# Optimization experiments

Hardware: AMD Instinct MI355X
Metric: run time of the kernel (lower is better)

## Reference

```python
import jax, jax.numpy as jnp
import numpy as np
from jax import lax

V, E, H = 32000, 32, 128
B, T = 8, 256


def setup_inputs() -> dict:
    key = jax.random.key(0)
    ks = jax.random.split(key, 10)
    inv = lambda n: 1.0 / np.sqrt(n)
    return {
        "x": jax.random.randint(ks[0], (B, T), 0, V, dtype=jnp.int32),
        "emb": jax.random.normal(ks[1], (V, E), dtype=jnp.float32),
        "W_attn": jax.random.normal(ks[2], (H, H), dtype=jnp.float32) * inv(H),   # attn_W weight
        "U_attn": jax.random.normal(ks[3], (H, H), dtype=jnp.float32) * inv(H),   # attn_U weight
        "v_attn": jax.random.normal(ks[4], (H,), dtype=jnp.float32) * inv(H),     # attn_v weight
        "W_ih": jax.random.normal(ks[5], (E + H, H), dtype=jnp.float32) * inv(E + H),
        "b_ih": jnp.zeros((H,), dtype=jnp.float32),
        "W_hh": jax.random.normal(ks[6], (H, H), dtype=jnp.float32) * inv(H),
        "b_hh": jnp.zeros((H,), dtype=jnp.float32),
        "W_out": jax.random.normal(ks[7], (H, V), dtype=jnp.float32) * inv(H),
        "b_out": jnp.zeros((V,), dtype=jnp.float32),
    }


def _run(x, emb, W_attn, U_attn, v_attn, W_ih, b_ih, W_hh, b_hh, W_out, b_out):
    Bb, Tt = x.shape
    Hh = W_hh.shape[0]
    embeds = jnp.swapaxes(emb[x], 0, 1)  # [T, B, E]
    t_idx = jnp.arange(Tt)

    def step(carry, inp):
        h, hid_buf = carry            # h: [B,H]; hid_buf: [T,B,H] (rows >= t are zeros)
        e_t, t = inp                  # e_t: [B,E]
        # Bahdanau attention over hidden states from steps < t
        q = h @ W_attn                                   # [B,H]
        keys = hid_buf @ U_attn                          # [T,B,H] (recomputed each step, as in source)
        energy = jnp.tanh(q[None, :, :] + keys)          # [T,B,H]
        scores = jnp.einsum('tbh,h->tb', energy, v_attn) # [T,B]
        valid = (jnp.arange(Tt) < t)[:, None]
        scores = jnp.where(valid, scores, -1e9)
        w = jax.nn.softmax(scores, axis=0)               # [T,B]
        ctx = jnp.einsum('tb,tbh->bh', w, hid_buf)       # [B,H]
        ctx = jnp.where(t > 0, ctx, jnp.zeros_like(ctx)) # t=0: zero context
        rnn_in = jnp.concatenate([e_t, ctx], axis=1)     # [B,E+H]
        h_new = jnp.tanh(rnn_in @ W_ih + b_ih + h @ W_hh + b_hh)
        hid_buf = hid_buf.at[t].set(h_new)
        return (h_new, hid_buf), h_new

    carry0 = (jnp.zeros((Bb, Hh), embeds.dtype), jnp.zeros((Tt, Bb, Hh), embeds.dtype))
    (h_final, _), outs = lax.scan(step, carry0, (embeds, t_idx))
    outputs = jnp.swapaxes(outs, 0, 1)                   # [B,T,H]
    logits = outputs @ W_out + b_out                     # [B,T,V]
    return logits, h_final


def reference(x, emb, W_attn, U_attn, v_attn, W_ih, b_ih, W_hh, b_hh, W_out, b_out):
    return _run(x, emb, W_attn, U_attn, v_attn, W_ih, b_ih, W_hh, b_hh, W_out, b_out)
```

## Files before the change

kernel.cpp:

```cpp
#include <hip/hip_runtime.h>
#include <hip/hip_fp16.h>
#include <hip/hip_bf16.h>
#include <cstdint>

#define TLEN  256
#define HD    128
#define BATCH 8
#define VOCAB 32000
#define EMBD  32
#define ROWB  272

typedef __attribute__((ext_vector_type(8))) short short8v;
typedef __attribute__((ext_vector_type(8))) unsigned short ushort8v;
typedef __attribute__((ext_vector_type(4))) float f32x4;
typedef __attribute__((ext_vector_type(2))) float f32x2;
typedef __attribute__((ext_vector_type(2))) _Float16 hv2;

__device__ __forceinline__ float tanhfast(float x){
  float e = __builtin_amdgcn_exp2f(x * 2.8853900817779268f);
  return 1.0f - 2.0f * __builtin_amdgcn_rcpf(e + 1.0f);
}
__device__ __forceinline__ unsigned short f2bf(float f){
  unsigned u = __float_as_uint(f);
  return (unsigned short)((u + 0x7fffu + ((u >> 16) & 1u)) >> 16);
}
__device__ __forceinline__ float h2f(unsigned short u){
  return __half2float(__ushort_as_half(u));
}
__device__ __forceinline__ unsigned short f2h(float f){
  return __half_as_ushort(__float2half(f));
}
__device__ __forceinline__ unsigned pk2(float lo, float hi){
  return __builtin_bit_cast(unsigned, __floats2half2_rn(lo, hi));
}
__device__ __forceinline__ float fdot2u(unsigned a, unsigned b, float c){
#if __has_builtin(__builtin_amdgcn_fdot2)
  return __builtin_amdgcn_fdot2(__builtin_bit_cast(hv2, a), __builtin_bit_cast(hv2, b), c, false);
#else
  float2 fa = __half22float2(__builtin_bit_cast(__half2, a));
  float2 fb = __half22float2(__builtin_bit_cast(__half2, b));
  return c + fa.x*fb.x + fa.y*fb.y;
#endif
}
__device__ __forceinline__ f32x2 fma2(f32x2 a, f32x2 b, f32x2 c){
#if __has_builtin(__builtin_elementwise_fma)
  return __builtin_elementwise_fma(a, b, c);
#else
  f32x2 r; r.x = fmaf(a.x, b.x, c.x); r.y = fmaf(a.y, b.y, c.y); return r;
#endif
}
__device__ __forceinline__ void ld8u(const void* p, unsigned* d){
  uint4 a = *(const uint4*)p;
  uint4 b = *(const uint4*)((const char*)p + 16);
  d[0]=a.x; d[1]=a.y; d[2]=a.z; d[3]=a.w; d[4]=b.x; d[5]=b.y; d[6]=b.z; d[7]=b.w;
}
__device__ __forceinline__ void gload_lds16(const void* g, void* l){
  __builtin_amdgcn_global_load_lds((const __attribute__((address_space(1))) void*)g,
                                   (__attribute__((address_space(3))) void*)l, 16, 0, 0);
}

__device__ __forceinline__ float dpp_add1(float x){
  int y = __builtin_amdgcn_mov_dpp(__float_as_int(x), 0xB1, 0xF, 0xF, true);
  return x + __int_as_float(y);
}
__device__ __forceinline__ float dpp_add2(float x){
  int y = __builtin_amdgcn_mov_dpp(__float_as_int(x), 0x4E, 0xF, 0xF, true);
  return x + __int_as_float(y);
}
__device__ __forceinline__ float dpp_shl4(float x){
  int y = __builtin_amdgcn_mov_dpp(__float_as_int(x), 0x104, 0xF, 0xF, true);
  return x + __int_as_float(y);
}
__device__ __forceinline__ float dpp_shl8(float x){
  int y = __builtin_amdgcn_mov_dpp(__float_as_int(x), 0x108, 0xF, 0xF, true);
  return x + __int_as_float(y);
}
__device__ __forceinline__ float swz_add4(float x){
  int y = __builtin_amdgcn_ds_swizzle(__float_as_int(x), 0x101F);
  return x + __int_as_float(y);
}
__device__ __forceinline__ float swz_add16(float x){
  int y = __builtin_amdgcn_ds_swizzle(__float_as_int(x), 0x401F);
  return x + __int_as_float(y);
}

#define SCR(s) ((((s) & 15) << 4) | ((s) >> 4))

__global__ void prep_ex_kernel(const int* __restrict__ x, const float* __restrict__ emb,
                               const float* __restrict__ W_ih, const float* __restrict__ b_ih,
                               const float* __restrict__ b_hh, float* __restrict__ ex){
  int bt = blockIdx.x;
  int c  = threadIdx.x;
  int ix = x[bt];
  const float* er = emb + (long)ix * EMBD;
  float acc = b_ih[c] + b_hh[c];
  #pragma unroll
  for (int e = 0; e < EMBD; ++e) acc += er[e] * W_ih[e * HD + c];
  ex[bt * HD + c] = acc;
}

__global__ void prep_wt_kernel(const float* __restrict__ W_out, unsigned short* __restrict__ Wbt){
  __shared__ float tile[32][33];
  int tx = threadIdx.x & 31, ty = threadIdx.x >> 5;
  int n0 = blockIdx.x * 32, k0 = blockIdx.y * 32;
  #pragma unroll
  for (int j = 0; j < 4; ++j){
    int k = ty + j * 8;
    tile[k][tx] = W_out[(long)(k0 + k) * VOCAB + n0 + tx];
  }
  __syncthreads();
  #pragma unroll
  for (int j = 0; j < 4; ++j){
    int n = ty + j * 8;
    Wbt[(long)(n0 + n) * HD + k0 + tx] = f2bf(tile[tx][n]);
  }
}

__launch_bounds__(1024)
__global__ void scan_kernel(const float* __restrict__ W_attn, const float* __restrict__ U_attn,
                            const float* __restrict__ v_attn, const float* __restrict__ W_ih,
                            const float* __restrict__ W_hh, const float* __restrict__ ex,
                            unsigned short* __restrict__ out_bf, float* __restrict__ h_final){
  extern __shared__ char lds[];
  char* keysB = lds;
  char* hWcB  = lds + 69632;
  float* fbuf   = (float*)(lds + 139264);
  float* E_pad    = fbuf;
  float* hh_lds   = fbuf + 160;
  float* scores_e = fbuf + 288;
  unsigned* h_pk  = (unsigned*)(fbuf + 544);

  const int b    = blockIdx.x;
  const int tid  = threadIdx.x;
  const int lane = tid & 63, wv = tid >> 6;
  const int c_   = tid >> 3, rg = tid & 7;
  const int sg   = lane >> 3, cg = lane & 7;
  const int cg3  = cg & 3;
  const int sgx  = sg + 8*(cg >> 2);
  const int cp   = wv*4 + cg3;

  const float LOG2E = 1.4426950408889634f;
  const float C2F   = 2.8853900817779268f;

  if (tid < HD) hh_lds[tid] = 0.f;

  unsigned Wa2[8], Ua2[8], Wh2[8], Wc2[8];
  {
    float* stage = (float*)lds;
    float4* d4 = (float4*)stage;
    {
      const float4* s4 = (const float4*)W_attn;
      for (int i = 0; i < 4; ++i) d4[tid + i*1024] = s4[tid + i*1024];
      __syncthreads();
      #pragma unroll
      for (int i = 0; i < 8; ++i)
        Wa2[i] = pk2(stage[(rg*16 + 2*i)*HD + c_], stage[(rg*16 + 2*i + 1)*HD + c_]);
      __syncthreads();
    }
    {
      const float4* s4 = (const float4*)U_attn;
      for (int i = 0; i < 4; ++i) d4[tid + i*1024] = s4[tid + i*1024];
      __syncthreads();
      #pragma unroll
      for (int i = 0; i < 8; ++i)
        Ua2[i] = pk2(stage[(rg*16 + 2*i)*HD + c_], stage[(rg*16 + 2*i + 1)*HD + c_]);
      __syncthreads();
    }
    {
      const float4* s4 = (const float4*)W_hh;
      for (int i = 0; i < 4; ++i) d4[tid + i*1024] = s4[tid + i*1024];
      __syncthreads();
      #pragma unroll
      for (int i = 0; i < 8; ++i)
        Wh2[i] = pk2(stage[(rg*16 + 2*i)*HD + c_], stage[(rg*16 + 2*i + 1)*HD + c_]);
      __syncthreads();
    }
    {
      const float4* s4 = (const float4*)(W_ih + EMBD*HD);
      for (int i = 0; i < 4; ++i) d4[tid + i*1024] = s4[tid + i*1024];
      __syncthreads();
      #pragma unroll
      for (int i = 0; i < 8; ++i)
        Wc2[i] = pk2(stage[(rg*16 + 2*i)*HD + c_], stage[(rg*16 + 2*i + 1)*HD + c_]);
      __syncthreads();
    }
  }

  {
    float4 z = {0.f, 0.f, 0.f, 0.f};
    float4* hz = (float4*)hWcB;
    hz[tid] = z; hz[tid + 1024] = z; hz[tid + 2048] = z; hz[tid + 3072] = z;
    if (tid < 256) hz[tid + 4096] = z;
    if (tid < 64) ((float4*)scores_e)[tid] = z;
    if (tid < 64) h_pk[tid] = 0u;
  }

  f32x2 v2[8]; float VsumL;
  {
    const float* vg = v_attn + cg*16;
    float s = 0.f;
    #pragma unroll
    for (int i = 0; i < 8; ++i){
      f32x2 vv; vv.x = vg[2*i]; vv.y = vg[2*i+1];
      v2[i] = vv; s += vv.x + vv.y;
    }
    s = dpp_add1(s); s = dpp_add2(s); s = swz_add4(s);
    VsumL = s * LOG2E;
  }

  const float* exb = ex + (long)b * TLEN * HD;

  for (int t = 0; t < TLEN; ++t){
    float2 evpre = *(const float2*)(exb + t*HD + 2*cp);

    if (t > 0){
      {
        unsigned h2u[8];
        ld8u((const char*)h_pk + rg*32, h2u);
        float aq = 0.f, ak = 0.f, ah = 0.f, aw = 0.f;
        #pragma unroll
        for (int i = 0; i < 8; ++i){
          aq = fdot2u(h2u[i], Wa2[i], aq);
          ak = fdot2u(h2u[i], Ua2[i], ak);
          ah = fdot2u(h2u[i], Wh2[i], ah);
          aw = fdot2u(h2u[i], Wc2[i], aw);
        }
        aq = dpp_add1(aq); aq = dpp_add2(aq); aq = dpp_shl4(aq);
        ak = dpp_add1(ak); ak = dpp_add2(ak); ak = dpp_shl4(ak);
        ah = dpp_add1(ah); ah = dpp_add2(ah); ah = dpp_shl4(ah);
        aw = dpp_add1(aw); aw = dpp_add2(aw); aw = dpp_shl4(aw);
        if (rg == 0){
          E_pad[c_ + (c_>>4)*4] = __builtin_amdgcn_exp2f(aq * C2F);
          hh_lds[c_] = ah;
          int s = t - 1;
          float G = fminf(__builtin_amdgcn_exp2f(ak * C2F), 60000.f);
          *(unsigned short*)(keysB + s*ROWB + c_*2) = f2h(G);
          *(unsigned short*)(hWcB  + s*ROWB + c_*2) = f2h(aw);
        }
      }
      __syncthreads();

      {
        f32x2 E2[8];
        {
          const float4* E4 = (const float4*)(E_pad + cg*20);
          #pragma unroll
          for (int i = 0; i < 4; ++i){
            float4 ev = E4[i];
            f32x2 a, bb; a.x = ev.x; a.y = ev.y; bb.x = ev.z; bb.y = ev.w;
            E2[2*i] = a; E2[2*i+1] = bb;
          }
        }
        #pragma unroll
        for (int it = 0; it < 2; ++it){
          int s = wv*8 + sg + it*128;
          if (s < t){
            unsigned gu[8];
            ld8u(keysB + s*ROWB + cg*32, gu);
            f32x2 D[8];
            #pragma unroll
            for (int i = 0; i < 8; ++i){
              hv2 g = __builtin_bit_cast(hv2, gu[i]);
              f32x2 d;
              d.x = fmaf((float)g.x, E2[i].x, 1.0f);
              d.y = fmaf((float)g.y, E2[i].y, 1.0f);
              D[i] = d;
            }
            f32x2 acc2; acc2.x = 0.f; acc2.y = 0.f;
            #pragma unroll
            for (int i = 0; i < 8; i += 2){
              f32x2 p = D[i] * D[i+1];
              float R = __builtin_amdgcn_rcpf(p.x * p.y);
              f32x2 sw = p.yx * R;
              acc2 = fma2(v2[i],   sw * D[i+1], acc2);
              acc2 = fma2(v2[i+1], sw * D[i],   acc2);
            }
            float ac = acc2.x + acc2.y;
            ac = dpp_add1(ac); ac = dpp_add2(ac); ac = dpp_shl4(ac);
            float e = __builtin_amdgcn_exp2f(fmaf(-C2F, ac, VsumL));
            if (cg == 0) scores_e[SCR(s)] = e;
          }
        }
      }
      __syncthreads();
    }

    {
      float a0 = 0.f, a1 = 0.f, es = 0.f;
      const char* pw = hWcB + cp*4 + sgx*ROWB;
      const float* sc = scores_e + sgx*16;
      int jmax = (t - sgx + 15) >> 4;
      for (int j = 0; j < jmax; j += 4){
        float4 e4 = *(const float4*)(sc + j);
        hv2 h0 = __builtin_bit_cast(hv2, *(const unsigned*)(pw));
        hv2 h1 = __builtin_bit_cast(hv2, *(const unsigned*)(pw + 16*ROWB));
        hv2 h2v = __builtin_bit_cast(hv2, *(const unsigned*)(pw + 32*ROWB));
        hv2 h3 = __builtin_bit_cast(hv2, *(const unsigned*)(pw + 48*ROWB));
        es += (e4.x + e4.y) + (e4.z + e4.w);
        a0 = fmaf((float)h0.x, e4.x, a0); a1 = fmaf((float)h0.y, e4.x, a1);
        a0 = fmaf((float)h1.x, e4.y, a0); a1 = fmaf((float)h1.y, e4.y, a1);
        a0 = fmaf((float)h2v.x, e4.z, a0); a1 = fmaf((float)h2v.y, e4.z, a1);
        a0 = fmaf((float)h3.x, e4.w, a0); a1 = fmaf((float)h3.y, e4.w, a1);
        pw += 64*ROWB;
      }
      a0 = dpp_shl4(a0); a0 = dpp_shl8(a0); a0 = swz_add16(a0); a0 += __shfl_xor(a0, 32);
      a1 = dpp_shl4(a1); a1 = dpp_shl8(a1); a1 = swz_add16(a1); a1 += __shfl_xor(a1, 32);
      es = dpp_shl4(es); es = dpp_shl8(es); es = swz_add16(es); es += __shfl_xor(es, 32);
      if (sgx == 0){
        float invZ = __builtin_amdgcn_rcpf(es);
        float cw0 = (t > 0) ? a0 * invZ : 0.f;
        float cw1 = (t > 0) ? a1 * invZ : 0.f;
        int c0 = 2*cp;
        float2 hhv = *(const float2*)(&hh_lds[c0]);
        float h0 = tanhfast(evpre.x + hhv.x + cw0);
        float h1 = tanhfast(evpre.y + hhv.y + cw1);
        h_pk[cp] = pk2(h0, h1);
        unsigned po = (unsigned)f2bf(h0) | ((unsigned)f2bf(h1) << 16);
        *(unsigned*)(&out_bf[((long)b*TLEN + t)*HD + c0]) = po;
        if (t == TLEN-1){ float2 hw = { h0, h1 }; *(float2*)&h_final[b*HD + c0] = hw; }
      }
    }
    __syncthreads();
  }
}

__launch_bounds__(256, 2)
__global__ void gemm_kernel(const unsigned short* __restrict__ A, const unsigned short* __restrict__ Bt,
                            const float* __restrict__ bias, float* __restrict__ C){
  __shared__ char sAB[65536];
  char* sA = sAB;
  char* sB = sAB + 32768;
  const int tid = threadIdx.x;
  const int lane = tid & 63, wv = tid >> 6;
  const int n0 = blockIdx.x * 128, m0 = blockIdx.y * 128;
  const char* Ab = (const char*)A + (long)m0 * 256;
  const char* Bb = (const char*)Bt + (long)n0 * 256;

  #pragma unroll
  for (int it = 0; it < 8; ++it){
    int p  = it*4096 + wv*1024 + lane*16;
    int ps = p ^ (((p >> 8) & 7) << 4);
    gload_lds16(Ab + ps, sA + it*4096 + wv*1024);
    gload_lds16(Bb + ps, sB + it*4096 + wv*1024);
  }
  __syncthreads();

  f32x4 acc[2][8] = {};
  const int r15 = lane & 15, r4 = lane >> 4;
  #pragma unroll
  for (int kk = 0; kk < 4; ++kk){
    short8v af[2], bfr[8];
    #pragma unroll
    for (int mi = 0; mi < 2; ++mi){
      int row = wv*32 + mi*16 + r15;
      int off = row*256 + kk*64 + r4*16;
      af[mi] = *(const short8v*)(sA + (off ^ ((row & 7) << 4)));
    }
    #pragma unroll
    for (int ni = 0; ni < 8; ++ni){
      int row = ni*16 + r15;
      int off = row*256 + kk*64 + r4*16;
      bfr[ni] = *(const short8v*)(sB + (off ^ ((row & 7) << 4)));
    }
    #pragma unroll
    for (int ni = 0; ni < 8; ++ni)
      #pragma unroll
      for (int mi = 0; mi < 2; ++mi)
        acc[mi][ni] = __builtin_amdgcn_mfma_f32_16x16x32_bf16(af[mi], bfr[ni], acc[mi][ni], 0, 0, 0);
  }

  #pragma unroll
  for (int mi = 0; mi < 2; ++mi){
    int rbase = m0 + wv*32 + mi*16 + r4*4;
    #pragma unroll
    for (int ni = 0; ni < 8; ++ni){
      int col = n0 + ni*16 + r15;
      float bv = bias[col];
      #pragma unroll
      for (int j = 0; j < 4; ++j)
        C[(long)(rbase + j) * VOCAB + col] = acc[mi][ni][j] + bv;
    }
  }
}

extern "C" void kernel_launch(void* const* d_in, const int* in_sizes, int n_in,
                              void* d_out, int out_size, void* d_ws, size_t ws_size,
                              hipStream_t stream){
  const int*   x      = (const int*)d_in[0];
  const float* emb    = (const float*)d_in[1];
  const float* W_attn = (const float*)d_in[2];
  const float* U_attn = (const float*)d_in[3];
  const float* v_attn = (const float*)d_in[4];
  const float* W_ih   = (const float*)d_in[5];
  const float* b_ih   = (const float*)d_in[6];
  const float* W_hh   = (const float*)d_in[7];
  const float* b_hh   = (const float*)d_in[8];
  const float* W_out  = (const float*)d_in[9];
  const float* b_out  = (const float*)d_in[10];

  float* logits  = (float*)d_out;
  float* h_final = logits + (long)BATCH * TLEN * VOCAB;

  char* ws = (char*)d_ws;
  float*          ex   = (float*)ws;
  unsigned short* Wbt  = (unsigned short*)(ws + 1048576);
  unsigned short* outb = (unsigned short*)(ws + 1048576 + 8192000);

  prep_ex_kernel<<<BATCH*TLEN, HD, 0, stream>>>(x, emb, W_ih, b_ih, b_hh, ex);
  prep_wt_kernel<<<dim3(VOCAB/32, HD/32), 256, 0, stream>>>(W_out, Wbt);

  const int ldsBytes = 139264 + 608*4;
  hipFuncSetAttribute((const void*)scan_kernel, hipFuncAttributeMaxDynamicSharedMemorySize, ldsBytes);
  scan_kernel<<<BATCH, 1024, ldsBytes, stream>>>(W_attn, U_attn, v_attn, W_ih, W_hh, ex, outb, h_final);

  gemm_kernel<<<dim3(VOCAB/128, (BATCH*TLEN)/128), 256, 0, stream>>>(outb, Wbt, b_out, logits);
}
```

Measured before the change: 650.2 us.

## Fuse scan and output GEMM into one persistent kernel with progress flags

Merges the recurrent scan and the vocabulary projection GEMM into a single launch. Eight blocks run the scan and publish per-batch progress every 64 steps via release atomics. Worker blocks poll these flags and compute GEMM tiles for rows that are already finished, so the large projection overlaps with the serial scan instead of waiting for it. The risks are deadlock if the scan blocks are not scheduled alongside spinning workers, and reduced GEMM efficiency because only 4 of 16 waves per 1024-thread worker block do the math and occupancy is limited by the large LDS allocation.

```diff
diff --git a/kernel.cpp b/kernel.cpp
--- a/kernel.cpp
+++ b/kernel.cpp
@@ -9,6 +9,7 @@
 #define VOCAB 32000
 #define EMBD  32
 #define ROWB  272
+#define NWORK 240
 
 typedef __attribute__((ext_vector_type(8))) short short8v;
 typedef __attribute__((ext_vector_type(8))) unsigned short ushort8v;
@@ -88,9 +89,11 @@
 
 __global__ void prep_ex_kernel(const int* __restrict__ x, const float* __restrict__ emb,
                                const float* __restrict__ W_ih, const float* __restrict__ b_ih,
-                               const float* __restrict__ b_hh, float* __restrict__ ex){
+                               const float* __restrict__ b_hh, float* __restrict__ ex,
+                               int* progress){
   int bt = blockIdx.x;
   int c  = threadIdx.x;
+  if (bt == 0 && c < BATCH) progress[c] = -1;
   int ix = x[bt];
   const float* er = emb + (long)ix * EMBD;
   float acc = b_ih[c] + b_hh[c];
@@ -116,12 +119,11 @@
   }
 }
 
-__launch_bounds__(1024)
-__global__ void scan_kernel(const float* __restrict__ W_attn, const float* __restrict__ U_attn,
-                            const float* __restrict__ v_attn, const float* __restrict__ W_ih,
-                            const float* __restrict__ W_hh, const float* __restrict__ ex,
-                            unsigned short* __restrict__ out_bf, float* __restrict__ h_final){
-  extern __shared__ char lds[];
+__device__ void scan_body(char* lds,
+                          const float* W_attn, const float* U_attn, const float* v_attn,
+                          const float* W_ih, const float* W_hh, const float* ex,
+                          unsigned short* out_bf, float* h_final, int* progress,
+                          int b, int tid){
   char* keysB = lds;
   char* hWcB  = lds + 69632;
   float* fbuf   = (float*)(lds + 139264);
@@ -130,8 +132,6 @@
   float* scores_e = fbuf + 288;
   unsigned* h_pk  = (unsigned*)(fbuf + 544);
 
-  const int b    = blockIdx.x;
-  const int tid  = threadIdx.x;
   const int lane = tid & 63, wv = tid >> 6;
   const int c_   = tid >> 3, rg = tid & 7;
   const int sg   = lane >> 3, cg = lane & 7;
@@ -321,65 +321,101 @@
       }
     }
     __syncthreads();
-  }
-}
-
-__launch_bounds__(256, 2)
-__global__ void gemm_kernel(const unsigned short* __restrict__ A, const unsigned short* __restrict__ Bt,
-                            const float* __restrict__ bias, float* __restrict__ C){
-  __shared__ char sAB[65536];
-  char* sA = sAB;
-  char* sB = sAB + 32768;
-  const int tid = threadIdx.x;
+
+    if (((t & 63) == 63) && tid == 0){
+      __threadfence();
+      __hip_atomic_store(&progress[b], t, __ATOMIC_RELEASE, __HIP_MEMORY_SCOPE_AGENT);
+    }
+  }
+}
+
+__device__ void worker_body(char* lds, const unsigned short* A, const unsigned short* Bt,
+                            const float* bias, float* C, int* progress, int wid, int tid){
+  char* sA = lds;
+  char* sB = lds + 32768;
   const int lane = tid & 63, wv = tid >> 6;
-  const int n0 = blockIdx.x * 128, m0 = blockIdx.y * 128;
-  const char* Ab = (const char*)A + (long)m0 * 256;
-  const char* Bb = (const char*)Bt + (long)n0 * 256;
-
-  #pragma unroll
-  for (int it = 0; it < 8; ++it){
-    int p  = it*4096 + wv*1024 + lane*16;
-    int ps = p ^ (((p >> 8) & 7) << 4);
-    gload_lds16(Ab + ps, sA + it*4096 + wv*1024);
-    gload_lds16(Bb + ps, sB + it*4096 + wv*1024);
-  }
-  __syncthreads();
-
-  f32x4 acc[2][8] = {};
   const int r15 = lane & 15, r4 = lane >> 4;
-  #pragma unroll
-  for (int kk = 0; kk < 4; ++kk){
-    short8v af[2], bfr[8];
-    #pragma unroll
-    for (int mi = 0; mi < 2; ++mi){
-      int row = wv*32 + mi*16 + r15;
-      int off = row*256 + kk*64 + r4*16;
-      af[mi] = *(const short8v*)(sA + (off ^ ((row & 7) << 4)));
-    }
-    #pragma unroll
-    for (int ni = 0; ni < 8; ++ni){
-      int row = ni*16 + r15;
-      int off = row*256 + kk*64 + r4*16;
-      bfr[ni] = *(const short8v*)(sB + (off ^ ((row & 7) << 4)));
-    }
-    #pragma unroll
-    for (int ni = 0; ni < 8; ++ni)
-      #pragma unroll
-      for (int mi = 0; mi < 2; ++mi)
-        acc[mi][ni] = __builtin_amdgcn_mfma_f32_16x16x32_bf16(af[mi], bfr[ni], acc[mi][ni], 0, 0, 0);
-  }
-
-  #pragma unroll
-  for (int mi = 0; mi < 2; ++mi){
-    int rbase = m0 + wv*32 + mi*16 + r4*4;
-    #pragma unroll
-    for (int ni = 0; ni < 8; ++ni){
-      int col = n0 + ni*16 + r15;
-      float bv = bias[col];
-      #pragma unroll
-      for (int j = 0; j < 4; ++j)
-        C[(long)(rbase + j) * VOCAB + col] = acc[mi][ni][j] + bv;
-    }
+
+  for (int tau = wid; tau < 4000; tau += NWORK){
+    int ph  = (tau >= 2000) ? 1 : 0;
+    int r   = tau - ph*2000;
+    int ni  = r >> 3;
+    int mi  = ((r & 7) << 1) + ph;
+    int bb  = mi >> 1;
+    int need = (mi & 1) ? 255 : 127;
+
+    if (tid == 0){
+      while (__hip_atomic_load(&progress[bb], __ATOMIC_ACQUIRE, __HIP_MEMORY_SCOPE_AGENT) < need)
+        __builtin_amdgcn_s_sleep(2);
+    }
+    __syncthreads();
+
+    const int n0 = ni * 128, m0 = mi * 128;
+    if (wv < 4){
+      const char* Ab = (const char*)A + (long)m0 * 256;
+      const char* Bb = (const char*)Bt + (long)n0 * 256;
+      #pragma unroll
+      for (int it = 0; it < 8; ++it){
+        int p  = it*4096 + wv*1024 + lane*16;
+        int ps = p ^ (((p >> 8) & 7) << 4);
+        gload_lds16(Ab + ps, sA + it*4096 + wv*1024);
+        gload_lds16(Bb + ps, sB + it*4096 + wv*1024);
+      }
+    }
+    __syncthreads();
+
+    if (wv < 4){
+      f32x4 acc[2][8] = {};
+      #pragma unroll
+      for (int kk = 0; kk < 4; ++kk){
+        short8v af[2], bfr[8];
+        #pragma unroll
+        for (int mi2 = 0; mi2 < 2; ++mi2){
+          int row = wv*32 + mi2*16 + r15;
+          int off = row*256 + kk*64 + r4*16;
+          af[mi2] = *(const short8v*)(sA + (off ^ ((row & 7) << 4)));
+        }
+        #pragma unroll
+        for (int ni2 = 0; ni2 < 8; ++ni2){
+          int row = ni2*16 + r15;
+          int off = row*256 + kk*64 + r4*16;
+          bfr[ni2] = *(const short8v*)(sB + (off ^ ((row & 7) << 4)));
+        }
+        #pragma unroll
+        for (int ni2 = 0; ni2 < 8; ++ni2)
+          #pragma unroll
+          for (int mi2 = 0; mi2 < 2; ++mi2)
+            acc[mi2][ni2] = __builtin_amdgcn_mfma_f32_16x16x32_bf16(af[mi2], bfr[ni2], acc[mi2][ni2], 0, 0, 0);
+      }
+      #pragma unroll
+      for (int mi2 = 0; mi2 < 2; ++mi2){
+        int rbase = m0 + wv*32 + mi2*16 + r4*4;
+        #pragma unroll
+        for (int ni2 = 0; ni2 < 8; ++ni2){
+          int col = n0 + ni2*16 + r15;
+          float bv = bias[col];
+          #pragma unroll
+          for (int j = 0; j < 4; ++j)
+            C[(long)(rbase + j) * VOCAB + col] = acc[mi2][ni2][j] + bv;
+        }
+      }
+    }
+    __syncthreads();
+  }
+}
+
+__launch_bounds__(1024)
+__global__ void fused_kernel(const float* W_attn, const float* U_attn, const float* v_attn,
+                             const float* W_ih, const float* W_hh, const float* ex,
+                             unsigned short* out_bf, float* h_final,
+                             const unsigned short* Bt, const float* bias, float* C,
+                             int* progress){
+  extern __shared__ char lds[];
+  if (blockIdx.x < BATCH){
+    scan_body(lds, W_attn, U_attn, v_attn, W_ih, W_hh, ex, out_bf, h_final, progress,
+              blockIdx.x, threadIdx.x);
+  } else {
+    worker_body(lds, out_bf, Bt, bias, C, progress, blockIdx.x - BATCH, threadIdx.x);
   }
 }
 
@@ -405,13 +441,13 @@
   float*          ex   = (float*)ws;
   unsigned short* Wbt  = (unsigned short*)(ws + 1048576);
   unsigned short* outb = (unsigned short*)(ws + 1048576 + 8192000);
-
-  prep_ex_kernel<<<BATCH*TLEN, HD, 0, stream>>>(x, emb, W_ih, b_ih, b_hh, ex);
+  int*            progress = (int*)(ws + 1048576 + 8192000 + 524288);
+
+  prep_ex_kernel<<<BATCH*TLEN, HD, 0, stream>>>(x, emb, W_ih, b_ih, b_hh, ex, progress);
   prep_wt_kernel<<<dim3(VOCAB/32, HD/32), 256, 0, stream>>>(W_out, Wbt);
 
   const int ldsBytes = 139264 + 608*4;
-  hipFuncSetAttribute((const void*)scan_kernel, hipFuncAttributeMaxDynamicSharedMemorySize, ldsBytes);
-  scan_kernel<<<BATCH, 1024, ldsBytes, stream>>>(W_attn, U_attn, v_attn, W_ih, W_hh, ex, outb, h_final);
-
-  gemm_kernel<<<dim3(VOCAB/128, (BATCH*TLEN)/128), 256, 0, stream>>>(outb, Wbt, b_out, logits);
-}
+  hipFuncSetAttribute((const void*)fused_kernel, hipFuncAttributeMaxDynamicSharedMemorySize, ldsBytes);
+  fused_kernel<<<BATCH + NWORK, 1024, ldsBytes, stream>>>(
+      W_attn, U_attn, v_attn, W_ih, W_hh, ex, outb, h_final, Wbt, b_out, logits, progress);
+}
```

Result: slower. 840.2 us (+29.2%).
